# Kernel tuning notes

Hardware: AMD Instinct MI355X
Metric: run time of the kernel (lower is better)

## Reference

```python
import jax, jax.numpy as jnp
import numpy as np

DIM = 1024
NUM_HEADS = 16
HEAD_DIM = DIM // NUM_HEADS


def setup_inputs() -> dict:
    key = jax.random.key(0)
    k1, k2, k3, k4, k5 = jax.random.split(key, 5)
    scale = 0.02
    return {
        "x": jax.random.normal(k1, (4, 2048, DIM), dtype=jnp.float32),
        "w_qkv": jax.random.normal(k2, (DIM, 3 * DIM), dtype=jnp.float32) * scale,
        "b_qkv": jax.random.normal(k3, (3 * DIM,), dtype=jnp.float32) * scale,
        "w_proj": jax.random.normal(k4, (DIM, DIM), dtype=jnp.float32) * scale,
        "b_proj": jax.random.normal(k5, (DIM,), dtype=jnp.float32) * scale,
    }


def reference(x, w_qkv, b_qkv, w_proj, b_proj):
    B, N, C = x.shape
    H, D = NUM_HEADS, HEAD_DIM
    qkv = x @ w_qkv + b_qkv                      # [B, N, 3C]
    qkv = qkv.reshape(B, N, 3, H, D)
    q = qkv[:, :, 0].transpose(0, 2, 1, 3)       # [B, H, N, D]
    k = qkv[:, :, 1].transpose(0, 2, 1, 3)
    v = qkv[:, :, 2].transpose(0, 2, 1, 3)
    attn = jnp.einsum("bhnd,bhmd->bhnm", q, k) / (D ** 0.5)  # [B, H, N, N]
    attn = jax.nn.softmax(attn, axis=-1)
    out = jnp.einsum("bhnm,bhmd->bhnd", attn, v)  # [B, H, N, D]
    out = out.transpose(0, 2, 1, 3).reshape(B, N, C)
    return out @ w_proj + b_proj
```

## Files before the change

kernel.cpp:

```cpp
#include <hip/hip_runtime.h>
#include <stdint.h>

typedef __bf16 bf16_t;
typedef __bf16 bf16x8 __attribute__((ext_vector_type(8)));
typedef __bf16 bf16x4 __attribute__((ext_vector_type(4)));
typedef float  f32x4  __attribute__((ext_vector_type(4)));

__device__ __forceinline__ void g2l16(const void* g, void* l) {
    __builtin_amdgcn_global_load_lds(
        (const __attribute__((address_space(1))) unsigned int*)g,
        (__attribute__((address_space(3))) unsigned int*)l, 16, 0, 0);
}

__global__ __launch_bounds__(256) void prep_kernel(
    const float* __restrict__ x, const float* __restrict__ w_qkv,
    const float* __restrict__ w_proj,
    bf16_t* __restrict__ x_bf, bf16_t* __restrict__ wqkvT, bf16_t* __restrict__ wprojT)
{
    __shared__ float t[32][33];
    const int bx = blockIdx.x;
    if (bx < 8192) {
        const int idx = (bx * 256 + threadIdx.x) * 4;
        const float4 v = *(const float4*)(x + idx);
        bf16x4 o;
        o[0] = (bf16_t)v.x; o[1] = (bf16_t)v.y; o[2] = (bf16_t)v.z; o[3] = (bf16_t)v.w;
        *(bf16x4*)(x_bf + idx) = o;
        return;
    }
    const float* in;
    bf16_t* outp;
    int c0, r0, C;
    if (bx < 11264) {
        const int b = bx - 8192;
        in = w_qkv; outp = wqkvT; C = 3072;
        c0 = (b % 96) * 32; r0 = (b / 96) * 32;
    } else {
        const int b = bx - 11264;
        in = w_proj; outp = wprojT; C = 1024;
        c0 = (b & 31) * 32; r0 = (b >> 5) * 32;
    }
    const int xx = threadIdx.x & 31, y = threadIdx.x >> 5;
    #pragma unroll
    for (int i = 0; i < 32; i += 8)
        t[y + i][xx] = in[(size_t)(r0 + y + i) * C + c0 + xx];
    __syncthreads();
    #pragma unroll
    for (int i = 0; i < 32; i += 8)
        outp[(size_t)(c0 + y + i) * 1024 + r0 + xx] = (bf16_t)t[xx][y + i];
}

__device__ __forceinline__ void gemm128(
    const bf16_t* __restrict__ A, const bf16_t* __restrict__ Bt, const int K,
    bf16_t* sA, bf16_t* sB, const int m0, const int n0, f32x4 acc[4][4])
{
    const int tid  = threadIdx.x;
    const int lane = tid & 63;
    const int w    = tid >> 6;
    const int wm   = (w >> 1) * 64;
    const int wn   = (w & 1) * 64;
    const int col0 = lane & 15;
    const int quad = lane >> 4;

    #pragma unroll
    for (int mt = 0; mt < 4; ++mt)
        #pragma unroll
        for (int nt = 0; nt < 4; ++nt)
            acc[mt][nt] = (f32x4){0.f, 0.f, 0.f, 0.f};

    const int srow = tid >> 3;
    const int jsw  = ((tid & 7) ^ (srow & 7)) << 3;
    const bf16_t* Ab = A  + (size_t)(m0 + srow) * K + jsw;
    const bf16_t* Bb = Bt + (size_t)(n0 + srow) * K + jsw;

    for (int kb = 0; kb < K; kb += 64) {
        #pragma unroll
        for (int it = 0; it < 4; ++it) {
            g2l16(Ab + (size_t)(it * 32) * K + kb, sA + (size_t)(it * 256 + tid) * 8);
            g2l16(Bb + (size_t)(it * 32) * K + kb, sB + (size_t)(it * 256 + tid) * 8);
        }
        __syncthreads();
        #pragma unroll
        for (int ks = 0; ks < 2; ++ks) {
            const int jg = ks * 4 + quad;
            bf16x8 af[4], bv[4];
            #pragma unroll
            for (int mt = 0; mt < 4; ++mt) {
                const int ra = wm + mt * 16 + col0;
                af[mt] = *(const bf16x8*)(sA + ra * 64 + ((jg ^ (ra & 7)) << 3));
            }
            #pragma unroll
            for (int nt = 0; nt < 4; ++nt) {
                const int rb = wn + nt * 16 + col0;
                bv[nt] = *(const bf16x8*)(sB + rb * 64 + ((jg ^ (rb & 7)) << 3));
            }
            #pragma unroll
            for (int mt = 0; mt < 4; ++mt)
                #pragma unroll
                for (int nt = 0; nt < 4; ++nt)
                    acc[mt][nt] = __builtin_amdgcn_mfma_f32_16x16x32_bf16(
                        af[mt], bv[nt], acc[mt][nt], 0, 0, 0);
        }
        __syncthreads();
    }
}

#define QSCALE 0.18033688f
__global__ __launch_bounds__(256) void qkv_gemm_kernel(
    const bf16_t* __restrict__ x, const bf16_t* __restrict__ wT,
    const float* __restrict__ bias,
    bf16_t* __restrict__ q, bf16_t* __restrict__ k, bf16_t* __restrict__ vT)
{
    __shared__ bf16_t sA[128 * 64];
    __shared__ bf16_t sB[128 * 64];
    const int m0 = blockIdx.y * 128;
    const int n0 = blockIdx.x * 128;
    f32x4 acc[4][4];
    gemm128(x, wT, 1024, sA, sB, m0, n0, acc);

    const int tid = threadIdx.x, lane = tid & 63, w = tid >> 6;
    const int wm = (w >> 1) * 64, wn = (w & 1) * 64;
    const int col0 = lane & 15, quad = lane >> 4;
    const int sel = n0 >> 10;

    #pragma unroll
    for (int mt = 0; mt < 4; ++mt) {
        const int m_base = m0 + wm + mt * 16 + quad * 4;
        const int b = m_base >> 11;
        const int t = m_base & 2047;
        #pragma unroll
        for (int nt = 0; nt < 4; ++nt) {
            const int n = n0 + wn + nt * 16 + col0;
            const float bvv = bias[n];
            const int h = (n >> 6) & 15, d = n & 63;
            const size_t bh = (size_t)b * 16 + h;
            if (sel == 0) {
                #pragma unroll
                for (int r = 0; r < 4; ++r)
                    q[(bh * 2048 + t + r) * 64 + d] = (bf16_t)((acc[mt][nt][r] + bvv) * QSCALE);
            } else if (sel == 1) {
                #pragma unroll
                for (int r = 0; r < 4; ++r)
                    k[(bh * 2048 + t + r) * 64 + d] = (bf16_t)(acc[mt][nt][r] + bvv);
            } else {
                #pragma unroll
                for (int r = 0; r < 4; ++r)
                    vT[(bh * 64 + d) * 2048 + t + r] = (bf16_t)(acc[mt][nt][r] + bvv);
            }
        }
    }
}

__global__ __launch_bounds__(256) void proj_gemm_kernel(
    const bf16_t* __restrict__ a, const bf16_t* __restrict__ wT,
    const float* __restrict__ bias, float* __restrict__ out)
{
    __shared__ bf16_t sA[128 * 64];
    __shared__ bf16_t sB[128 * 64];
    const int m0 = blockIdx.y * 128;
    const int n0 = blockIdx.x * 128;
    f32x4 acc[4][4];
    gemm128(a, wT, 1024, sA, sB, m0, n0, acc);

    const int tid = threadIdx.x, lane = tid & 63, w = tid >> 6;
    const int wm = (w >> 1) * 64, wn = (w & 1) * 64;
    const int col0 = lane & 15, quad = lane >> 4;
    #pragma unroll
    for (int mt = 0; mt < 4; ++mt) {
        const int m_base = m0 + wm + mt * 16 + quad * 4;
        #pragma unroll
        for (int nt = 0; nt < 4; ++nt) {
            const int n = n0 + wn + nt * 16 + col0;
            const float bvv = bias[n];
            #pragma unroll
            for (int r = 0; r < 4; ++r)
                out[(size_t)(m_base + r) * 1024 + n] = acc[mt][nt][r] + bvv;
        }
    }
}

__global__ __launch_bounds__(256, 4) void attn_kernel(
    const bf16_t* __restrict__ q, const bf16_t* __restrict__ k,
    const bf16_t* __restrict__ vT, bf16_t* __restrict__ out)
{
    __shared__ __align__(16) char smem[16384 + 16384];
    bf16_t* sK = (bf16_t*)smem;
    bf16_t* sV = (bf16_t*)(smem + 16384);

    const int x   = blockIdx.x;
    const int loc = x >> 3;
    const int qb  = loc & 15;
    const int bh  = (x & 7) + ((loc >> 4) << 3);

    const int tid = threadIdx.x, lane = tid & 63, w = tid >> 6;
    const int col0 = lane & 15, quad = lane >> 4;

    const bf16_t* qbase = q  + ((size_t)bh * 2048 + qb * 128) * 64;
    const bf16_t* kbase = k  + (size_t)bh * 2048 * 64;
    const bf16_t* vbase = vT + (size_t)bh * 64 * 2048;

    const int srow8  = tid >> 3;
    const int jsw8   = ((tid & 7) ^ (srow8 & 7)) << 3;
    const int srow16 = tid >> 4;
    const int jsw16  = ((tid & 15) ^ (srow16 & 15)) << 3;

    bf16x8 qf[2][2];
    #pragma unroll
    for (int mt = 0; mt < 2; ++mt)
        #pragma unroll
        for (int ks = 0; ks < 2; ++ks)
            qf[mt][ks] = *(const bf16x8*)(qbase
                + (size_t)(w * 32 + mt * 16 + col0) * 64 + ks * 32 + quad * 8);

    f32x4 oacc[2][4];
    float row_l[2];
    #pragma unroll
    for (int mt = 0; mt < 2; ++mt) {
        #pragma unroll
        for (int nt = 0; nt < 4; ++nt) oacc[mt][nt] = (f32x4){0.f, 0.f, 0.f, 0.f};
        row_l[mt] = 0.f;
    }

    for (int kv = 0; kv < 16; ++kv) {
        const bf16_t* kg = kbase + (size_t)kv * 128 * 64;
        #pragma unroll
        for (int it = 0; it < 4; ++it)
            g2l16(kg + (size_t)(it * 32 + srow8) * 64 + jsw8,
                  sK + (size_t)(it * 256 + tid) * 8);
        #pragma unroll
        for (int it = 0; it < 4; ++it)
            g2l16(vbase + (size_t)(it * 16 + srow16) * 2048 + kv * 128 + jsw16,
                  sV + (size_t)(it * 256 + tid) * 8);
        __syncthreads();

        #pragma unroll
        for (int hf = 0; hf < 2; ++hf) {
            f32x4 s[4][2];
            #pragma unroll
            for (int nt = 0; nt < 4; ++nt)
                #pragma unroll
                for (int mt = 0; mt < 2; ++mt) s[nt][mt] = (f32x4){0.f, 0.f, 0.f, 0.f};
            #pragma unroll
            for (int ks = 0; ks < 2; ++ks) {
                const int jg = ks * 4 + quad;
                bf16x8 kf[4];
                #pragma unroll
                for (int nt = 0; nt < 4; ++nt) {
                    const int rk = hf * 64 + nt * 16 + col0;
                    kf[nt] = *(const bf16x8*)(sK + rk * 64 + ((jg ^ (rk & 7)) << 3));
                }
                #pragma unroll
                for (int nt = 0; nt < 4; ++nt)
                    #pragma unroll
                    for (int mt = 0; mt < 2; ++mt)
                        s[nt][mt] = __builtin_amdgcn_mfma_f32_16x16x32_bf16(
                            kf[nt], qf[mt][ks], s[nt][mt], 0, 0, 0);
            }

            #pragma unroll
            for (int kp = 0; kp < 2; ++kp) {
                const int jg2 = (hf * 2 + kp) * 4 + quad;
                bf16x8 vf[4];
                #pragma unroll
                for (int nt = 0; nt < 4; ++nt) {
                    const int dv = nt * 16 + col0;
                    vf[nt] = *(const bf16x8*)(sV + dv * 128 + ((jg2 ^ (dv & 15)) << 3));
                }
                #pragma unroll
                for (int mt = 0; mt < 2; ++mt) {
                    float p0[4], p1[4];
                    float rs = 0.f;
                    #pragma unroll
                    for (int r = 0; r < 4; ++r) {
                        p0[r] = __builtin_amdgcn_exp2f(s[2 * kp][mt][r]);
                        p1[r] = __builtin_amdgcn_exp2f(s[2 * kp + 1][mt][r]);
                        rs += p0[r] + p1[r];
                    }
                    row_l[mt] += rs;
                    unsigned XA, XB, YA, YB;
                    asm("v_cvt_pk_bf16_f32 %0, %1, %2" : "=v"(XA) : "v"(p0[0]), "v"(p0[1]));
                    asm("v_cvt_pk_bf16_f32 %0, %1, %2" : "=v"(XB) : "v"(p0[2]), "v"(p0[3]));
                    asm("v_cvt_pk_bf16_f32 %0, %1, %2" : "=v"(YA) : "v"(p1[0]), "v"(p1[1]));
                    asm("v_cvt_pk_bf16_f32 %0, %1, %2" : "=v"(YB) : "v"(p1[2]), "v"(p1[3]));
                    asm("v_permlane32_swap_b32 %0, %1" : "+v"(XA), "+v"(YA));
                    asm("v_permlane16_swap_b32 %0, %1" : "+v"(XA), "+v"(YA));
                    asm("v_permlane32_swap_b32 %0, %1" : "+v"(XB), "+v"(YB));
                    asm("v_permlane16_swap_b32 %0, %1" : "+v"(XB), "+v"(YB));
                    union { unsigned wds[4]; bf16x8 v; } u;
                    u.wds[0] = XA; u.wds[1] = XB; u.wds[2] = YA; u.wds[3] = YB;
                    #pragma unroll
                    for (int nt = 0; nt < 4; ++nt)
                        oacc[mt][nt] = __builtin_amdgcn_mfma_f32_16x16x32_bf16(
                            u.v, vf[nt], oacc[mt][nt], 0, 0, 0);
                }
            }
        }
        __syncthreads();
    }

    float lt[2];
    #pragma unroll
    for (int mt = 0; mt < 2; ++mt) {
        float l = row_l[mt];
        l += __shfl_xor(l, 16);
        l += __shfl_xor(l, 32);
        lt[mt] = l;
    }
    const int b = bh >> 4, h = bh & 15;
    #pragma unroll
    for (int mt = 0; mt < 2; ++mt) {
        #pragma unroll
        for (int r = 0; r < 4; ++r) {
            const float inv = 1.0f / __shfl(lt[mt], quad * 4 + r);
            const int t = qb * 128 + w * 32 + mt * 16 + quad * 4 + r;
            const size_t rowbase = ((size_t)b * 2048 + t) * 1024 + h * 64;
            #pragma unroll
            for (int nt = 0; nt < 4; ++nt)
                out[rowbase + nt * 16 + col0] = (bf16_t)(oacc[mt][nt][r] * inv);
        }
    }
}

extern "C" void kernel_launch(void* const* d_in, const int* in_sizes, int n_in,
                              void* d_out, int out_size, void* d_ws, size_t ws_size,
                              hipStream_t stream) {
    const float* x      = (const float*)d_in[0];
    const float* w_qkv  = (const float*)d_in[1];
    const float* b_qkv  = (const float*)d_in[2];
    const float* w_proj = (const float*)d_in[3];
    const float* b_proj = (const float*)d_in[4];
    float* out = (float*)d_out;

    char* p = (char*)d_ws;
    bf16_t* x_bf   = (bf16_t*)p; p += (size_t)8192 * 1024 * 2;
    bf16_t* wqkvT  = (bf16_t*)p; p += (size_t)3072 * 1024 * 2;
    bf16_t* wprojT = (bf16_t*)p; p += (size_t)1024 * 1024 * 2;
    bf16_t* qb     = (bf16_t*)p; p += (size_t)8192 * 1024 * 2;
    bf16_t* kb     = (bf16_t*)p; p += (size_t)8192 * 1024 * 2;
    bf16_t* vTb    = (bf16_t*)p; p += (size_t)8192 * 1024 * 2;
    bf16_t* attb   = (bf16_t*)p; p += (size_t)8192 * 1024 * 2;

    prep_kernel<<<12288, 256, 0, stream>>>(x, w_qkv, w_proj, x_bf, wqkvT, wprojT);
    qkv_gemm_kernel<<<dim3(24, 64), 256, 0, stream>>>(x_bf, wqkvT, b_qkv, qb, kb, vTb);
    attn_kernel<<<1024, 256, 0, stream>>>(qb, kb, vTb, attb);
    proj_gemm_kernel<<<dim3(8, 64), 256, 0, stream>>>(attb, wprojT, b_proj, out);
}
```

Before: 271.2 us.

## Register-prefetch next K/V tile in attention loop with smaller 64-key tiles

The attention kernel drops the direct global-to-LDS loads of 128-key K/V tiles. It now stages 64-key tiles through registers, issuing the global loads for the next tile before computing on the current one so memory latency overlaps with MFMA work. Shared memory per block is halved, and s_setprio brackets the MFMA sequences to favour matrix issue. In exchange there are twice as many loop iterations and barriers, plus extra VGPRs for the prefetch buffers, which may limit occupancy.

Result: slower. 284.4 us (+4.9%).

```diff
diff --git a/kernel.cpp b/kernel.cpp
--- a/kernel.cpp
+++ b/kernel.cpp
@@ -182,9 +182,9 @@
     const bf16_t* __restrict__ q, const bf16_t* __restrict__ k,
     const bf16_t* __restrict__ vT, bf16_t* __restrict__ out)
 {
-    __shared__ __align__(16) char smem[16384 + 16384];
+    __shared__ __align__(16) char smem[16384];
     bf16_t* sK = (bf16_t*)smem;
-    bf16_t* sV = (bf16_t*)(smem + 16384);
+    bf16_t* sV = (bf16_t*)(smem + 8192);
 
     const int x   = blockIdx.x;
     const int loc = x >> 3;
@@ -198,10 +198,8 @@
     const bf16_t* kbase = k  + (size_t)bh * 2048 * 64;
     const bf16_t* vbase = vT + (size_t)bh * 64 * 2048;
 
-    const int srow8  = tid >> 3;
-    const int jsw8   = ((tid & 7) ^ (srow8 & 7)) << 3;
-    const int srow16 = tid >> 4;
-    const int jsw16  = ((tid & 15) ^ (srow16 & 15)) << 3;
+    const int srow8 = tid >> 3;
+    const int jsw8  = ((tid & 7) ^ (srow8 & 7)) << 3;
 
     bf16x8 qf[2][2];
     #pragma unroll
@@ -211,6 +209,13 @@
             qf[mt][ks] = *(const bf16x8*)(qbase
                 + (size_t)(w * 32 + mt * 16 + col0) * 64 + ks * 32 + quad * 8);
 
+    bf16x8 kr[2], vr[2];
+    #pragma unroll
+    for (int it = 0; it < 2; ++it) {
+        kr[it] = *(const bf16x8*)(kbase + (size_t)(it * 32 + srow8) * 64 + jsw8);
+        vr[it] = *(const bf16x8*)(vbase + (size_t)(it * 32 + srow8) * 2048 + jsw8);
+    }
+
     f32x4 oacc[2][4];
     float row_l[2];
     #pragma unroll
@@ -220,81 +225,90 @@
         row_l[mt] = 0.f;
     }
 
-    for (int kv = 0; kv < 16; ++kv) {
-        const bf16_t* kg = kbase + (size_t)kv * 128 * 64;
-        #pragma unroll
-        for (int it = 0; it < 4; ++it)
-            g2l16(kg + (size_t)(it * 32 + srow8) * 64 + jsw8,
-                  sK + (size_t)(it * 256 + tid) * 8);
-        #pragma unroll
-        for (int it = 0; it < 4; ++it)
-            g2l16(vbase + (size_t)(it * 16 + srow16) * 2048 + kv * 128 + jsw16,
-                  sV + (size_t)(it * 256 + tid) * 8);
+    for (int t = 0; t < 32; ++t) {
         __syncthreads();
-
-        #pragma unroll
-        for (int hf = 0; hf < 2; ++hf) {
-            f32x4 s[4][2];
+        #pragma unroll
+        for (int it = 0; it < 2; ++it)
+            *(bf16x8*)(sK + (size_t)(it * 256 + tid) * 8) = kr[it];
+        #pragma unroll
+        for (int it = 0; it < 2; ++it)
+            *(bf16x8*)(sV + (size_t)(it * 256 + tid) * 8) = vr[it];
+        __syncthreads();
+
+        if (t < 31) {
+            #pragma unroll
+            for (int it = 0; it < 2; ++it)
+                kr[it] = *(const bf16x8*)(kbase
+                    + (size_t)((t + 1) * 64 + it * 32 + srow8) * 64 + jsw8);
+            #pragma unroll
+            for (int it = 0; it < 2; ++it)
+                vr[it] = *(const bf16x8*)(vbase
+                    + (size_t)(it * 32 + srow8) * 2048 + (t + 1) * 64 + jsw8);
+        }
+
+        f32x4 s[4][2];
+        #pragma unroll
+        for (int nt = 0; nt < 4; ++nt)
+            #pragma unroll
+            for (int mt = 0; mt < 2; ++mt) s[nt][mt] = (f32x4){0.f, 0.f, 0.f, 0.f};
+        #pragma unroll
+        for (int ks = 0; ks < 2; ++ks) {
+            const int jg = ks * 4 + quad;
+            bf16x8 kf[4];
+            #pragma unroll
+            for (int nt = 0; nt < 4; ++nt) {
+                const int rk = nt * 16 + col0;
+                kf[nt] = *(const bf16x8*)(sK + rk * 64 + ((jg ^ (rk & 7)) << 3));
+            }
+            __builtin_amdgcn_s_setprio(1);
             #pragma unroll
             for (int nt = 0; nt < 4; ++nt)
                 #pragma unroll
-                for (int mt = 0; mt < 2; ++mt) s[nt][mt] = (f32x4){0.f, 0.f, 0.f, 0.f};
-            #pragma unroll
-            for (int ks = 0; ks < 2; ++ks) {
-                const int jg = ks * 4 + quad;
-                bf16x8 kf[4];
-                #pragma unroll
-                for (int nt = 0; nt < 4; ++nt) {
-                    const int rk = hf * 64 + nt * 16 + col0;
-                    kf[nt] = *(const bf16x8*)(sK + rk * 64 + ((jg ^ (rk & 7)) << 3));
+                for (int mt = 0; mt < 2; ++mt)
+                    s[nt][mt] = __builtin_amdgcn_mfma_f32_16x16x32_bf16(
+                        kf[nt], qf[mt][ks], s[nt][mt], 0, 0, 0);
+            __builtin_amdgcn_s_setprio(0);
+        }
+
+        #pragma unroll
+        for (int kp = 0; kp < 2; ++kp) {
+            const int jj = kp * 4 + quad;
+            bf16x8 vf[4];
+            #pragma unroll
+            for (int nt = 0; nt < 4; ++nt) {
+                const int dv = nt * 16 + col0;
+                vf[nt] = *(const bf16x8*)(sV + dv * 64 + ((jj ^ (dv & 7)) << 3));
+            }
+            #pragma unroll
+            for (int mt = 0; mt < 2; ++mt) {
+                float p0[4], p1[4];
+                float rs = 0.f;
+                #pragma unroll
+                for (int r = 0; r < 4; ++r) {
+                    p0[r] = __builtin_amdgcn_exp2f(s[2 * kp][mt][r]);
+                    p1[r] = __builtin_amdgcn_exp2f(s[2 * kp + 1][mt][r]);
+                    rs += p0[r] + p1[r];
                 }
+                row_l[mt] += rs;
+                unsigned XA, XB, YA, YB;
+                asm("v_cvt_pk_bf16_f32 %0, %1, %2" : "=v"(XA) : "v"(p0[0]), "v"(p0[1]));
+                asm("v_cvt_pk_bf16_f32 %0, %1, %2" : "=v"(XB) : "v"(p0[2]), "v"(p0[3]));
+                asm("v_cvt_pk_bf16_f32 %0, %1, %2" : "=v"(YA) : "v"(p1[0]), "v"(p1[1]));
+                asm("v_cvt_pk_bf16_f32 %0, %1, %2" : "=v"(YB) : "v"(p1[2]), "v"(p1[3]));
+                asm("v_permlane32_swap_b32 %0, %1" : "+v"(XA), "+v"(YA));
+                asm("v_permlane16_swap_b32 %0, %1" : "+v"(XA), "+v"(YA));
+                asm("v_permlane32_swap_b32 %0, %1" : "+v"(XB), "+v"(YB));
+                asm("v_permlane16_swap_b32 %0, %1" : "+v"(XB), "+v"(YB));
+                union { unsigned wds[4]; bf16x8 v; } u;
+                u.wds[0] = XA; u.wds[1] = XB; u.wds[2] = YA; u.wds[3] = YB;
+                __builtin_amdgcn_s_setprio(1);
                 #pragma unroll
                 for (int nt = 0; nt < 4; ++nt)
-                    #pragma unroll
-                    for (int mt = 0; mt < 2; ++mt)
-                        s[nt][mt] = __builtin_amdgcn_mfma_f32_16x16x32_bf16(
-                            kf[nt], qf[mt][ks], s[nt][mt], 0, 0, 0);
-            }
-
-            #pragma unroll
-            for (int kp = 0; kp < 2; ++kp) {
-                const int jg2 = (hf * 2 + kp) * 4 + quad;
-                bf16x8 vf[4];
-                #pragma unroll
-                for (int nt = 0; nt < 4; ++nt) {
-                    const int dv = nt * 16 + col0;
-                    vf[nt] = *(const bf16x8*)(sV + dv * 128 + ((jg2 ^ (dv & 15)) << 3));
-                }
-                #pragma unroll
-                for (int mt = 0; mt < 2; ++mt) {
-                    float p0[4], p1[4];
-                    float rs = 0.f;
-                    #pragma unroll
-                    for (int r = 0; r < 4; ++r) {
-                        p0[r] = __builtin_amdgcn_exp2f(s[2 * kp][mt][r]);
-                        p1[r] = __builtin_amdgcn_exp2f(s[2 * kp + 1][mt][r]);
-                        rs += p0[r] + p1[r];
-                    }
-                    row_l[mt] += rs;
-                    unsigned XA, XB, YA, YB;
-                    asm("v_cvt_pk_bf16_f32 %0, %1, %2" : "=v"(XA) : "v"(p0[0]), "v"(p0[1]));
-                    asm("v_cvt_pk_bf16_f32 %0, %1, %2" : "=v"(XB) : "v"(p0[2]), "v"(p0[3]));
-                    asm("v_cvt_pk_bf16_f32 %0, %1, %2" : "=v"(YA) : "v"(p1[0]), "v"(p1[1]));
-                    asm("v_cvt_pk_bf16_f32 %0, %1, %2" : "=v"(YB) : "v"(p1[2]), "v"(p1[3]));
-                    asm("v_permlane32_swap_b32 %0, %1" : "+v"(XA), "+v"(YA));
-                    asm("v_permlane16_swap_b32 %0, %1" : "+v"(XA), "+v"(YA));
-                    asm("v_permlane32_swap_b32 %0, %1" : "+v"(XB), "+v"(YB));
-                    asm("v_permlane16_swap_b32 %0, %1" : "+v"(XB), "+v"(YB));
-                    union { unsigned wds[4]; bf16x8 v; } u;
-                    u.wds[0] = XA; u.wds[1] = XB; u.wds[2] = YA; u.wds[3] = YB;
-                    #pragma unroll
-                    for (int nt = 0; nt < 4; ++nt)
-                        oacc[mt][nt] = __builtin_amdgcn_mfma_f32_16x16x32_bf16(
-                            u.v, vf[nt], oacc[mt][nt], 0, 0, 0);
-                }
-            }
-        }
-        __syncthreads();
+                    oacc[mt][nt] = __builtin_amdgcn_mfma_f32_16x16x32_bf16(
+                        u.v, vf[nt], oacc[mt][nt], 0, 0, 0);
+                __builtin_amdgcn_s_setprio(0);
+            }
+        }
     }
 
     float lt[2];
```
